# Performance work log

Hardware: AMD Instinct MI355X
Metric: run time of the kernel (lower is better)

Reference implementation:

```python
import math
import jax, jax.numpy as jnp
import numpy as np

EMBED_DIM = 192
N_HEADS = 6
WS = 7          # window size (hardcoded by RelativeEmbedding's 13x13 table)
HW = 56         # spatial height = width (N = 56*56 = 3136)
BATCH = 32
NW = HW // WS   # windows per side = 8
WW = WS * WS    # tokens per window = 49


def _rel_indices():
    # Replicates the from-scratch Swin RelativeEmbedding index construction:
    # x = arange(1, 8, 1/7); xi = trunc(x[None]-x[:,None]); y = tile(arange(1,8), 7)
    xs = np.arange(1.0, 8.0, 1.0 / 7.0)          # 49 values
    xi = (xs[None, :] - xs[:, None]).astype(np.int32)  # trunc toward zero, in [-6, 6]
    ys = np.concatenate([np.arange(1, 8)] * 7)
    yi = (ys[None, :] - ys[:, None]).astype(np.int32)
    # torch negative indexing wraps -> emulate with mod 13
    return jnp.asarray(xi % 13), jnp.asarray(yi % 13)


def _masks():
    half = WS * (WS // 2)  # 21
    mm = np.zeros((WW, WW), dtype=np.float32)
    mm[-half:, :-half] = -np.inf
    mm[:-half, -half:] = -np.inf
    # cross_mask = rearrange(mm, '(r w1) (c w2) -> (w1 r) (w2 c)')
    cross = mm.reshape(WS, WS, WS, WS).transpose(1, 0, 3, 2).reshape(WW, WW)
    return jnp.asarray(mm), jnp.asarray(cross)


def setup_inputs() -> dict:
    key = jax.random.key(0)
    ks = jax.random.split(key, 6)
    return {
        "x": jax.random.normal(ks[0], (BATCH, HW * HW, EMBED_DIM), jnp.float32),
        "W_qkv": jax.random.normal(ks[1], (3 * EMBED_DIM, EMBED_DIM), jnp.float32) * 0.02,
        "b_qkv": jax.random.normal(ks[2], (3 * EMBED_DIM,), jnp.float32) * 0.02,
        "W_out": jax.random.normal(ks[3], (EMBED_DIM, EMBED_DIM), jnp.float32) * 0.02,
        "b_out": jax.random.normal(ks[4], (EMBED_DIM,), jnp.float32) * 0.02,
        "B_rel": jax.random.normal(ks[5], (2 * WS - 1, 2 * WS - 1), jnp.float32),
    }


def reference(x, W_qkv, b_qkv, W_out, b_out, B_rel):
    B = x.shape[0]
    hd = EMBED_DIM // N_HEADS
    xi, yi = _rel_indices()
    bias = B_rel[xi, yi]                      # (49, 49) relative position bias
    mm, cross = _masks()

    qkv = x @ W_qkv.T + b_qkv                 # (B, N, 3E)
    # 'b (h w) (c k) -> b h w c k' : channel-major, k fastest
    qkv = qkv.reshape(B, HW, HW, EMBED_DIM, 3)
    # shifted windows: source uses -window_size // 2 == -4 (asymmetric w/ reverse +3)
    qkv = jnp.roll(qkv, shift=(-(WS) // 2, -(WS) // 2), axis=(1, 2))
    # 'b (h m1) (w m2) (H E) K -> b H h w (m1 m2) E K'
    qkv = qkv.reshape(B, NW, WS, NW, WS, N_HEADS, hd, 3)
    qkv = qkv.transpose(0, 5, 1, 3, 2, 4, 6, 7).reshape(B, N_HEADS, NW, NW, WW, hd, 3)
    q, k, v = qkv[..., 0], qkv[..., 1], qkv[..., 2]

    scores = jnp.einsum('bHhwie,bHhwje->bHhwij', q, k) / math.sqrt(hd)
    scores = scores + bias                    # broadcast over (b, H, h, w)
    # shift masking: last row of windows and last column of windows
    scores = scores.at[:, :, -1, :].add(mm)
    scores = scores.at[:, :, :, -1].add(cross)

    p = jax.nn.softmax(scores, axis=-1)
    out = jnp.einsum('bHhwij,bHhwje->bHhwie', p, v)  # (B, H, nw, nw, 49, hd)
    # 'b H h w (m1 m2) E -> b (h m1) (w m2) (H E)'
    out = out.reshape(B, N_HEADS, NW, NW, WS, WS, hd)
    out = out.transpose(0, 2, 4, 3, 5, 1, 6).reshape(B, HW, HW, EMBED_DIM)
    out = jnp.roll(out, shift=(WS // 2, WS // 2), axis=(1, 2))
    out = out.reshape(B, HW * HW, EMBED_DIM)
    return out @ W_out.T + b_out
```

## Files before the change

### kernel.cpp

```cpp
#include <hip/hip_runtime.h>

typedef _Float16 f16;
typedef _Float16 f16x4 __attribute__((ext_vector_type(4)));
typedef _Float16 f16x8 __attribute__((ext_vector_type(8)));
typedef float f32x4 __attribute__((ext_vector_type(4)));

#define MFMA32(A, B, C) __builtin_amdgcn_mfma_f32_16x16x32_f16((A), (B), (C), 0, 0, 0)
#if __has_builtin(__builtin_amdgcn_mfma_f32_16x16x16_f16)
#define MFMA16(A, B, C) __builtin_amdgcn_mfma_f32_16x16x16_f16((A), (B), (C), 0, 0, 0)
#else
#define MFMA16(A, B, C) __builtin_amdgcn_mfma_f32_16x16x16f16((A), (B), (C), 0, 0, 0)
#endif

__global__ void prep_kernel(const float* __restrict__ Wq, const float* __restrict__ bqkv,
                            const float* __restrict__ Wo, const float* __restrict__ Brel,
                            f16* __restrict__ wqd, f16* __restrict__ wod,
                            float* __restrict__ bqd, f16* __restrict__ biasreg) {
  int tid = blockIdx.x * blockDim.x + threadIdx.x;
  int nthr = gridDim.x * blockDim.x;
  for (int i = tid; i < 3 * 192 * 192; i += nthr) {
    int c = i % 192, n = (i / 192) % 192, kk = i / (192 * 192);
    wqd[i] = (f16)Wq[(size_t)(n * 3 + kk) * 192 + c];
  }
  for (int i = tid; i < 192 * 192; i += nthr) wod[i] = (f16)Wo[i];
  for (int i = tid; i < 3 * 192; i += nthr) {
    int n = i % 192, kk = i / 192;
    bqd[i] = bqkv[n * 3 + kk];
  }
  for (int idx = tid; idx < 4 * 4 * 4 * 64 * 4; idx += nthr) {
    int m = idx & 3, lane = (idx >> 2) & 63, jt = (idx >> 8) & 3,
        itt = (idx >> 10) & 3, t = idx >> 12;
    int i = itt * 16 + (lane & 15);
    int j = jt * 16 + 4 * (lane >> 4) + m;
    float v = -60000.0f;
    if (i < 49 && j < 49) {
      bool msk = false;
      if (t & 2) msk |= ((i / 7 >= 4) != (j / 7 >= 4));
      if (t & 1) msk |= ((i % 7 >= 4) != (j % 7 >= 4));
      if (!msk) {
        volatile double one = 1.0;
        volatile double step = 1.0 / 7.0;
        volatile double b1 = one + step;
        volatile double delta = b1 - one;
        volatile double mj = (double)j * delta;
        volatile double sj = 1.0 + mj;
        volatile double mi = (double)i * delta;
        volatile double si = 1.0 + mi;
        double d = (double)sj - (double)si;
        int xd = (int)d;
        int yd = (j % 7) - (i % 7);
        int xm = ((xd % 13) + 13) % 13;
        int ym = ((yd % 13) + 13) % 13;
        v = Brel[xm * 13 + ym];
      }
    }
    biasreg[idx] = (f16)v;
  }
}

__launch_bounds__(768, 3)
__global__ void swin_kernel(const float* __restrict__ x,
                            const float* __restrict__ bqd,
                            const float* __restrict__ bout,
                            const f16* __restrict__ wqd,
                            const f16* __restrict__ wod,
                            const f16* __restrict__ biasreg,
                            float* __restrict__ out) {
  __shared__ __align__(16) unsigned char xsm[2 * 64 * 384];

  const int tid = threadIdx.x;
  const int bid = blockIdx.x;
  const int p  = bid >> 6;
  const int wh = (bid >> 3) & 7;
  const int ww = bid & 7;
  const int lane = tid & 63;
  const int wv = tid >> 6;
  const int t  = (wv >= 6) ? 1 : 0;
  const int hd = wv - 6 * t;
  const int lr = lane & 15;
  const int lg = lane >> 4;

#define XP(tt, row, cb) ((void*)(xsm + (tt) * 24576 + (row) * 384 + ((cb) ^ (((row) & 7) << 4))))

  {
    for (int idx = tid; idx < 2 * 49 * 48; idx += 768) {
      int tw = idx / (49 * 48), r = idx % (49 * 48);
      int tok = r / 48, c4 = r % 48;
      const float* xb = x + (size_t)(2 * p + tw) * (3136 * 192);
      int m1 = tok / 7, m2 = tok % 7;
      int y  = wh * 7 + m1 + 4; if (y  >= 56) y  -= 56;
      int xx = ww * 7 + m2 + 4; if (xx >= 56) xx -= 56;
      float4 v = *(const float4*)(xb + ((y * 56 + xx) * 192 + c4 * 4));
      f16x4 h = { (f16)v.x, (f16)v.y, (f16)v.z, (f16)v.w };
      *(f16x4*)XP(tw, tok, c4 * 8) = h;
    }
    for (int idx = tid; idx < 2 * 15 * 24; idx += 768) {
      int tw = idx / (15 * 24), r = idx % (15 * 24);
      int tok = 49 + r / 24, c8 = r % 24;
      f16x8 z = {};
      *(f16x8*)XP(tw, tok, c8 * 16) = z;
    }
  }
  __syncthreads();

  f16x4 br[4][4];
  {
    int msk = ((wh == 7) ? 2 : 0) | ((ww == 7) ? 1 : 0);
    #pragma unroll
    for (int itt = 0; itt < 4; ++itt)
      #pragma unroll
      for (int jt = 0; jt < 4; ++jt)
        br[itt][jt] = *(const f16x4*)(biasreg + ((((msk * 4 + itt) * 4 + jt) * 64 + lane) * 4));
  }

  f16x4 qtf[2][4], ktf[2][4];
  {
    f32x4 qacc[2][4], kacc[2][4];
    #pragma unroll
    for (int nt = 0; nt < 2; ++nt)
      #pragma unroll
      for (int it = 0; it < 4; ++it) {
        qacc[nt][it] = (f32x4){0.f, 0.f, 0.f, 0.f};
        kacc[nt][it] = (f32x4){0.f, 0.f, 0.f, 0.f};
      }
    #pragma unroll
    for (int ks = 0; ks < 6; ++ks) {
      f16x8 a[4];
      #pragma unroll
      for (int it = 0; it < 4; ++it)
        a[it] = *(const f16x8*)XP(t, it * 16 + lr, ks * 64 + lg * 16);
      #pragma unroll
      for (int nt = 0; nt < 2; ++nt) {
        const size_t roff = (size_t)(hd * 32 + nt * 16 + lr) * 192 + ks * 32 + lg * 8;
        f16x8 wqf = *(const f16x8*)(wqd + roff);
        f16x8 wkf = *(const f16x8*)(wqd + 192 * 192 + roff);
        #pragma unroll
        for (int it = 0; it < 4; ++it) {
          qacc[nt][it] = MFMA32(wqf, a[it], qacc[nt][it]);
          kacc[nt][it] = MFMA32(wkf, a[it], kacc[nt][it]);
        }
      }
    }
    const float SCALE = 0.17677669529663687f;
    #pragma unroll
    for (int nt = 0; nt < 2; ++nt) {
      float4 bq4 = *(const float4*)(bqd + hd * 32 + nt * 16 + 4 * lg);
      float4 bk4 = *(const float4*)(bqd + 192 + hd * 32 + nt * 16 + 4 * lg);
      #pragma unroll
      for (int it = 0; it < 4; ++it) {
        f16x4 q, k;
        q[0] = (f16)((qacc[nt][it][0] + bq4.x) * SCALE);
        q[1] = (f16)((qacc[nt][it][1] + bq4.y) * SCALE);
        q[2] = (f16)((qacc[nt][it][2] + bq4.z) * SCALE);
        q[3] = (f16)((qacc[nt][it][3] + bq4.w) * SCALE);
        k[0] = (f16)(kacc[nt][it][0] + bk4.x);
        k[1] = (f16)(kacc[nt][it][1] + bk4.y);
        k[2] = (f16)(kacc[nt][it][2] + bk4.z);
        k[3] = (f16)(kacc[nt][it][3] + bk4.w);
        qtf[nt][it] = q; ktf[nt][it] = k;
      }
    }
  }

  f32x4 sacc[4][4];
  #pragma unroll
  for (int jt = 0; jt < 4; ++jt)
    #pragma unroll
    for (int it = 0; it < 4; ++it) {
      f32x4 c = (f32x4){0.f, 0.f, 0.f, 0.f};
      c = MFMA16(ktf[0][jt], qtf[0][it], c);
      sacc[jt][it] = MFMA16(ktf[1][jt], qtf[1][it], c);
    }

  f16x4 paf[4][4];
  #pragma unroll
  for (int itt = 0; itt < 4; ++itt) {
    float sv[16];
    #pragma unroll
    for (int jt = 0; jt < 4; ++jt)
      #pragma unroll
      for (int m = 0; m < 4; ++m)
        sv[jt * 4 + m] = sacc[jt][itt][m] + (float)br[itt][jt][m];
    float mx = sv[0];
    #pragma unroll
    for (int q = 1; q < 16; ++q) mx = fmaxf(mx, sv[q]);
    mx = fmaxf(mx, __shfl_xor(mx, 16));
    mx = fmaxf(mx, __shfl_xor(mx, 32));
    float sum = 0.f;
    #pragma unroll
    for (int q = 0; q < 16; ++q) { sv[q] = __expf(sv[q] - mx); sum += sv[q]; }
    sum += __shfl_xor(sum, 16);
    sum += __shfl_xor(sum, 32);
    float rv = 1.0f / sum;
    #pragma unroll
    for (int jt = 0; jt < 4; ++jt) {
      f16x4 pk = { (f16)(sv[jt*4+0] * rv), (f16)(sv[jt*4+1] * rv),
                   (f16)(sv[jt*4+2] * rv), (f16)(sv[jt*4+3] * rv) };
      paf[jt][itt] = pk;
    }
  }

  f16x4 vf[4][2];
  {
    f32x4 vacc[4][2];
    #pragma unroll
    for (int jt = 0; jt < 4; ++jt)
      #pragma unroll
      for (int et = 0; et < 2; ++et)
        vacc[jt][et] = (f32x4){0.f, 0.f, 0.f, 0.f};
    #pragma unroll
    for (int ks = 0; ks < 6; ++ks) {
      f16x8 a[4];
      #pragma unroll
      for (int jt = 0; jt < 4; ++jt)
        a[jt] = *(const f16x8*)XP(t, jt * 16 + lr, ks * 64 + lg * 16);
      #pragma unroll
      for (int et = 0; et < 2; ++et) {
        f16x8 wvf = *(const f16x8*)(wqd + 2 * 192 * 192 +
                      (size_t)(hd * 32 + et * 16 + lr) * 192 + ks * 32 + lg * 8);
        #pragma unroll
        for (int jt = 0; jt < 4; ++jt)
          vacc[jt][et] = MFMA32(a[jt], wvf, vacc[jt][et]);
      }
    }
    #pragma unroll
    for (int et = 0; et < 2; ++et) {
      float bv = bqd[2 * 192 + hd * 32 + et * 16 + lr];
      #pragma unroll
      for (int jt = 0; jt < 4; ++jt) {
        f16x4 v;
        #pragma unroll
        for (int m = 0; m < 4; ++m) v[m] = (f16)(vacc[jt][et][m] + bv);
        vf[jt][et] = v;
      }
    }
  }

  f32x4 oacc[4][2];
  #pragma unroll
  for (int it = 0; it < 4; ++it)
    #pragma unroll
    for (int et = 0; et < 2; ++et) {
      f32x4 c = (f32x4){0.f, 0.f, 0.f, 0.f};
      #pragma unroll
      for (int jt = 0; jt < 4; ++jt)
        c = MFMA16(paf[jt][it], vf[jt][et], c);
      oacc[it][et] = c;
    }

  __syncthreads();

  #pragma unroll
  for (int it = 0; it < 4; ++it)
    #pragma unroll
    for (int et = 0; et < 2; ++et)
      #pragma unroll
      for (int m = 0; m < 4; ++m) {
        int i = it * 16 + 4 * lg + m;
        *(f16*)XP(t, i, hd * 64 + et * 32 + lr * 2) = (f16)(oacc[it][et][m]);
      }
  __syncthreads();

  f32x4 zacc[2][4];
  {
    #pragma unroll
    for (int nt = 0; nt < 2; ++nt)
      #pragma unroll
      for (int it = 0; it < 4; ++it)
        zacc[nt][it] = (f32x4){0.f, 0.f, 0.f, 0.f};
    #pragma unroll
    for (int ks = 0; ks < 6; ++ks) {
      f16x8 a[4];
      #pragma unroll
      for (int it = 0; it < 4; ++it)
        a[it] = *(const f16x8*)XP(t, it * 16 + lr, ks * 64 + lg * 16);
      #pragma unroll
      for (int nt = 0; nt < 2; ++nt) {
        f16x8 bw = *(const f16x8*)(wod + (size_t)(hd * 32 + nt * 16 + lr) * 192 + ks * 32 + lg * 8);
        #pragma unroll
        for (int it = 0; it < 4; ++it)
          zacc[nt][it] = MFMA32(a[it], bw, zacc[nt][it]);
      }
    }
  }
  __syncthreads();

  #pragma unroll
  for (int nt = 0; nt < 2; ++nt) {
    int n = hd * 32 + nt * 16 + lr;
    float bo = bout[n];
    #pragma unroll
    for (int it = 0; it < 4; ++it)
      #pragma unroll
      for (int m = 0; m < 4; ++m) {
        int i = it * 16 + 4 * lg + m;
        *(f16*)XP(t, i, n * 2) = (f16)(zacc[nt][it][m] + bo);
      }
  }
  __syncthreads();

  {
    for (int idx = tid; idx < 2 * 49 * 48; idx += 768) {
      int tw = idx / (49 * 48), r = idx % (49 * 48);
      int tok = r / 48, c4 = r % 48;
      float* outb = out + (size_t)(2 * p + tw) * (3136 * 192);
      f16x4 z = *(const f16x4*)XP(tw, tok, c4 * 8);
      int m1 = tok / 7, m2 = tok % 7;
      int y  = wh * 7 + m1 + 3; if (y  >= 56) y  -= 56;
      int xx = ww * 7 + m2 + 3; if (xx >= 56) xx -= 56;
      float4 v = { (float)z[0], (float)z[1], (float)z[2], (float)z[3] };
      *(float4*)(outb + (size_t)(y * 56 + xx) * 192 + c4 * 4) = v;
    }
  }
#undef XP
}

extern "C" void kernel_launch(void* const* d_in, const int* in_sizes, int n_in,
                              void* d_out, int out_size, void* d_ws, size_t ws_size,
                              hipStream_t stream) {
  const float* x    = (const float*)d_in[0];
  const float* Wq   = (const float*)d_in[1];
  const float* bq   = (const float*)d_in[2];
  const float* Wo   = (const float*)d_in[3];
  const float* bo   = (const float*)d_in[4];
  const float* Brel = (const float*)d_in[5];

  f16*   wqd     = (f16*)d_ws;
  f16*   wod     = (f16*)((char*)d_ws + 0x38000);
  float* bqd     = (float*)((char*)d_ws + 0x4A000);
  f16*   biasreg = (f16*)((char*)d_ws + 0x4B000);

  hipLaunchKernelGGL(prep_kernel, dim3(256), dim3(256), 0, stream,
                     Wq, bq, Wo, Brel, wqd, wod, bqd, biasreg);
  hipLaunchKernelGGL(swin_kernel, dim3(16 * 8 * 8), dim3(768), 0, stream,
                     x, bqd, bo, wqd, wod, biasreg, (float*)d_out);
}
```

Baseline: 155.7 us.

## Warp-specialize swin kernel with dedicated load/store waves double-buffering window pairs

The grid is reduced to 256 persistent-style blocks of 1024 threads. Each block handles four image pairs for one window position. Twelve compute waves run attention, while four extra waves store the previous pair's output and prefetch the next pair into a second LDS buffer. Global loads and stores also become nontemporal. The aim is to hide the gather/scatter memory latency behind MFMA work, at the cost of double the LDS (96KB per block), fewer blocks in flight, and the matching __syncthreads counts that the producer waves rely on.

```diff
diff --git a/kernel.cpp b/kernel.cpp
--- a/kernel.cpp
+++ b/kernel.cpp
@@ -58,7 +58,7 @@
   }
 }
 
-__launch_bounds__(768, 3)
+__launch_bounds__(1024, 4)
 __global__ void swin_kernel(const float* __restrict__ x,
                             const float* __restrict__ bqd,
                             const float* __restrict__ bout,
@@ -66,41 +66,63 @@
                             const f16* __restrict__ wod,
                             const f16* __restrict__ biasreg,
                             float* __restrict__ out) {
-  __shared__ __align__(16) unsigned char xsm[2 * 64 * 384];
+  __shared__ __align__(16) unsigned char xsm[4 * 64 * 384];
 
   const int tid = threadIdx.x;
   const int bid = blockIdx.x;
-  const int p  = bid >> 6;
   const int wh = (bid >> 3) & 7;
   const int ww = bid & 7;
+  const int g  = bid >> 6;
   const int lane = tid & 63;
   const int wv = tid >> 6;
-  const int t  = (wv >= 6) ? 1 : 0;
-  const int hd = wv - 6 * t;
+  const bool isC = (wv < 12);
+  const int t  = (isC && wv >= 6) ? 1 : 0;
+  const int hd = isC ? (wv - 6 * t) : 0;
   const int lr = lane & 15;
   const int lg = lane >> 4;
+  const int mid = (wv - 12) * 64 + lane;
 
 #define XP(tt, row, cb) ((void*)(xsm + (tt) * 24576 + (row) * 384 + ((cb) ^ (((row) & 7) << 4))))
 
-  {
-    for (int idx = tid; idx < 2 * 49 * 48; idx += 768) {
-      int tw = idx / (49 * 48), r = idx % (49 * 48);
-      int tok = r / 48, c4 = r % 48;
-      const float* xb = x + (size_t)(2 * p + tw) * (3136 * 192);
-      int m1 = tok / 7, m2 = tok % 7;
-      int y  = wh * 7 + m1 + 4; if (y  >= 56) y  -= 56;
-      int xx = ww * 7 + m2 + 4; if (xx >= 56) xx -= 56;
-      float4 v = *(const float4*)(xb + ((y * 56 + xx) * 192 + c4 * 4));
-      f16x4 h = { (f16)v.x, (f16)v.y, (f16)v.z, (f16)v.w };
-      *(f16x4*)XP(tw, tok, c4 * 8) = h;
-    }
-    for (int idx = tid; idx < 2 * 15 * 24; idx += 768) {
-      int tw = idx / (15 * 24), r = idx % (15 * 24);
-      int tok = 49 + r / 24, c8 = r % 24;
-      f16x8 z = {};
-      *(f16x8*)XP(tw, tok, c8 * 16) = z;
-    }
-  }
+#define STAGE(pr, st, base, stride)                                              \
+  {                                                                              \
+    for (int idx = (base); idx < 4704; idx += (stride)) {                        \
+      int tw = idx / 2352, r = idx % 2352;                                       \
+      int tok = r / 48, c4 = r % 48;                                             \
+      const float* xb = x + (size_t)(2 * (pr) + tw) * (3136 * 192);              \
+      int m1 = tok / 7, m2 = tok % 7;                                            \
+      int y  = wh * 7 + m1 + 4; if (y  >= 56) y  -= 56;                          \
+      int xx = ww * 7 + m2 + 4; if (xx >= 56) xx -= 56;                          \
+      f32x4 v = __builtin_nontemporal_load(                                      \
+          (const f32x4*)(xb + ((y * 56 + xx) * 192 + c4 * 4)));                  \
+      f16x4 h = { (f16)v[0], (f16)v[1], (f16)v[2], (f16)v[3] };                  \
+      *(f16x4*)XP((st) * 2 + tw, tok, c4 * 8) = h;                               \
+    }                                                                            \
+    for (int idx = (base); idx < 720; idx += (stride)) {                         \
+      int tw = idx / 360, r = idx % 360;                                         \
+      int tok = 49 + r / 24, c8 = r % 24;                                        \
+      f16x8 z = {};                                                              \
+      *(f16x8*)XP((st) * 2 + tw, tok, c8 * 16) = z;                              \
+    }                                                                            \
+  }
+
+#define EPILOGUE(pr, st, base, stride)                                           \
+  {                                                                              \
+    for (int idx = (base); idx < 4704; idx += (stride)) {                        \
+      int tw = idx / 2352, r = idx % 2352;                                       \
+      int tok = r / 48, c4 = r % 48;                                             \
+      float* outb = out + (size_t)(2 * (pr) + tw) * (3136 * 192);                \
+      f16x4 z = *(const f16x4*)XP((st) * 2 + tw, tok, c4 * 8);                   \
+      int m1 = tok / 7, m2 = tok % 7;                                            \
+      int y  = wh * 7 + m1 + 3; if (y  >= 56) y  -= 56;                          \
+      int xx = ww * 7 + m2 + 3; if (xx >= 56) xx -= 56;                          \
+      f32x4 v = { (float)z[0], (float)z[1], (float)z[2], (float)z[3] };          \
+      __builtin_nontemporal_store(v,                                             \
+          (f32x4*)(outb + (size_t)(y * 56 + xx) * 192 + c4 * 4));                \
+    }                                                                            \
+  }
+
+  STAGE(g * 4, 0, tid, 1024)
   __syncthreads();
 
   f16x4 br[4][4];
@@ -113,206 +135,210 @@
         br[itt][jt] = *(const f16x4*)(biasreg + ((((msk * 4 + itt) * 4 + jt) * 64 + lane) * 4));
   }
 
-  f16x4 qtf[2][4], ktf[2][4];
-  {
-    f32x4 qacc[2][4], kacc[2][4];
-    #pragma unroll
-    for (int nt = 0; nt < 2; ++nt)
-      #pragma unroll
-      for (int it = 0; it < 4; ++it) {
-        qacc[nt][it] = (f32x4){0.f, 0.f, 0.f, 0.f};
-        kacc[nt][it] = (f32x4){0.f, 0.f, 0.f, 0.f};
-      }
-    #pragma unroll
-    for (int ks = 0; ks < 6; ++ks) {
-      f16x8 a[4];
+  for (int w = 0; w < 4; ++w) {
+    const int S = w & 1;
+    const int tt = S * 2 + t;
+
+    if (isC) {
+      f16x4 qtf[2][4], ktf[2][4];
+      {
+        f32x4 qacc[2][4], kacc[2][4];
+        #pragma unroll
+        for (int nt = 0; nt < 2; ++nt)
+          #pragma unroll
+          for (int it = 0; it < 4; ++it) {
+            qacc[nt][it] = (f32x4){0.f, 0.f, 0.f, 0.f};
+            kacc[nt][it] = (f32x4){0.f, 0.f, 0.f, 0.f};
+          }
+        #pragma unroll
+        for (int ks = 0; ks < 6; ++ks) {
+          f16x8 a[4];
+          #pragma unroll
+          for (int it = 0; it < 4; ++it)
+            a[it] = *(const f16x8*)XP(tt, it * 16 + lr, ks * 64 + lg * 16);
+          #pragma unroll
+          for (int nt = 0; nt < 2; ++nt) {
+            const size_t roff = (size_t)(hd * 32 + nt * 16 + lr) * 192 + ks * 32 + lg * 8;
+            f16x8 wqf = *(const f16x8*)(wqd + roff);
+            f16x8 wkf = *(const f16x8*)(wqd + 192 * 192 + roff);
+            #pragma unroll
+            for (int it = 0; it < 4; ++it) {
+              qacc[nt][it] = MFMA32(wqf, a[it], qacc[nt][it]);
+              kacc[nt][it] = MFMA32(wkf, a[it], kacc[nt][it]);
+            }
+          }
+        }
+        const float SCALE = 0.17677669529663687f;
+        #pragma unroll
+        for (int nt = 0; nt < 2; ++nt) {
+          float4 bq4 = *(const float4*)(bqd + hd * 32 + nt * 16 + 4 * lg);
+          float4 bk4 = *(const float4*)(bqd + 192 + hd * 32 + nt * 16 + 4 * lg);
+          #pragma unroll
+          for (int it = 0; it < 4; ++it) {
+            f16x4 q, k;
+            q[0] = (f16)((qacc[nt][it][0] + bq4.x) * SCALE);
+            q[1] = (f16)((qacc[nt][it][1] + bq4.y) * SCALE);
+            q[2] = (f16)((qacc[nt][it][2] + bq4.z) * SCALE);
+            q[3] = (f16)((qacc[nt][it][3] + bq4.w) * SCALE);
+            k[0] = (f16)(kacc[nt][it][0] + bk4.x);
+            k[1] = (f16)(kacc[nt][it][1] + bk4.y);
+            k[2] = (f16)(kacc[nt][it][2] + bk4.z);
+            k[3] = (f16)(kacc[nt][it][3] + bk4.w);
+            qtf[nt][it] = q; ktf[nt][it] = k;
+          }
+        }
+      }
+
+      f32x4 sacc[4][4];
+      #pragma unroll
+      for (int jt = 0; jt < 4; ++jt)
+        #pragma unroll
+        for (int it = 0; it < 4; ++it) {
+          f32x4 c = (f32x4){0.f, 0.f, 0.f, 0.f};
+          c = MFMA16(ktf[0][jt], qtf[0][it], c);
+          sacc[jt][it] = MFMA16(ktf[1][jt], qtf[1][it], c);
+        }
+
+      f16x4 paf[4][4];
+      #pragma unroll
+      for (int itt = 0; itt < 4; ++itt) {
+        float sv[16];
+        #pragma unroll
+        for (int jt = 0; jt < 4; ++jt)
+          #pragma unroll
+          for (int m = 0; m < 4; ++m)
+            sv[jt * 4 + m] = sacc[jt][itt][m] + (float)br[itt][jt][m];
+        float mx = sv[0];
+        #pragma unroll
+        for (int q = 1; q < 16; ++q) mx = fmaxf(mx, sv[q]);
+        mx = fmaxf(mx, __shfl_xor(mx, 16));
+        mx = fmaxf(mx, __shfl_xor(mx, 32));
+        float sum = 0.f;
+        #pragma unroll
+        for (int q = 0; q < 16; ++q) { sv[q] = __expf(sv[q] - mx); sum += sv[q]; }
+        sum += __shfl_xor(sum, 16);
+        sum += __shfl_xor(sum, 32);
+        float rv = 1.0f / sum;
+        #pragma unroll
+        for (int jt = 0; jt < 4; ++jt) {
+          f16x4 pk = { (f16)(sv[jt*4+0] * rv), (f16)(sv[jt*4+1] * rv),
+                       (f16)(sv[jt*4+2] * rv), (f16)(sv[jt*4+3] * rv) };
+          paf[jt][itt] = pk;
+        }
+      }
+
+      f16x4 vf[4][2];
+      {
+        f32x4 vacc[4][2];
+        #pragma unroll
+        for (int jt = 0; jt < 4; ++jt)
+          #pragma unroll
+          for (int et = 0; et < 2; ++et)
+            vacc[jt][et] = (f32x4){0.f, 0.f, 0.f, 0.f};
+        #pragma unroll
+        for (int ks = 0; ks < 6; ++ks) {
+          f16x8 a[4];
+          #pragma unroll
+          for (int jt = 0; jt < 4; ++jt)
+            a[jt] = *(const f16x8*)XP(tt, jt * 16 + lr, ks * 64 + lg * 16);
+          #pragma unroll
+          for (int et = 0; et < 2; ++et) {
+            f16x8 wvf = *(const f16x8*)(wqd + 2 * 192 * 192 +
+                          (size_t)(hd * 32 + et * 16 + lr) * 192 + ks * 32 + lg * 8);
+            #pragma unroll
+            for (int jt = 0; jt < 4; ++jt)
+              vacc[jt][et] = MFMA32(a[jt], wvf, vacc[jt][et]);
+          }
+        }
+        #pragma unroll
+        for (int et = 0; et < 2; ++et) {
+          float bv = bqd[2 * 192 + hd * 32 + et * 16 + lr];
+          #pragma unroll
+          for (int jt = 0; jt < 4; ++jt) {
+            f16x4 v;
+            #pragma unroll
+            for (int m = 0; m < 4; ++m) v[m] = (f16)(vacc[jt][et][m] + bv);
+            vf[jt][et] = v;
+          }
+        }
+      }
+
+      f32x4 oacc[4][2];
       #pragma unroll
       for (int it = 0; it < 4; ++it)
-        a[it] = *(const f16x8*)XP(t, it * 16 + lr, ks * 64 + lg * 16);
+        #pragma unroll
+        for (int et = 0; et < 2; ++et) {
+          f32x4 c = (f32x4){0.f, 0.f, 0.f, 0.f};
+          #pragma unroll
+          for (int jt = 0; jt < 4; ++jt)
+            c = MFMA16(paf[jt][it], vf[jt][et], c);
+          oacc[it][et] = c;
+        }
+
+      __syncthreads();
+
+      #pragma unroll
+      for (int it = 0; it < 4; ++it)
+        #pragma unroll
+        for (int et = 0; et < 2; ++et)
+          #pragma unroll
+          for (int m = 0; m < 4; ++m) {
+            int i = it * 16 + 4 * lg + m;
+            *(f16*)XP(tt, i, hd * 64 + et * 32 + lr * 2) = (f16)(oacc[it][et][m]);
+          }
+      __syncthreads();
+
+      f32x4 zacc[2][4];
+      {
+        #pragma unroll
+        for (int nt = 0; nt < 2; ++nt)
+          #pragma unroll
+          for (int it = 0; it < 4; ++it)
+            zacc[nt][it] = (f32x4){0.f, 0.f, 0.f, 0.f};
+        #pragma unroll
+        for (int ks = 0; ks < 6; ++ks) {
+          f16x8 a[4];
+          #pragma unroll
+          for (int it = 0; it < 4; ++it)
+            a[it] = *(const f16x8*)XP(tt, it * 16 + lr, ks * 64 + lg * 16);
+          #pragma unroll
+          for (int nt = 0; nt < 2; ++nt) {
+            f16x8 bw = *(const f16x8*)(wod + (size_t)(hd * 32 + nt * 16 + lr) * 192 + ks * 32 + lg * 8);
+            #pragma unroll
+            for (int it = 0; it < 4; ++it)
+              zacc[nt][it] = MFMA32(a[it], bw, zacc[nt][it]);
+          }
+        }
+      }
+      __syncthreads();
+
       #pragma unroll
       for (int nt = 0; nt < 2; ++nt) {
-        const size_t roff = (size_t)(hd * 32 + nt * 16 + lr) * 192 + ks * 32 + lg * 8;
-        f16x8 wqf = *(const f16x8*)(wqd + roff);
-        f16x8 wkf = *(const f16x8*)(wqd + 192 * 192 + roff);
-        #pragma unroll
-        for (int it = 0; it < 4; ++it) {
-          qacc[nt][it] = MFMA32(wqf, a[it], qacc[nt][it]);
-          kacc[nt][it] = MFMA32(wkf, a[it], kacc[nt][it]);
-        }
-      }
+        int n = hd * 32 + nt * 16 + lr;
+        float bo = bout[n];
+        #pragma unroll
+        for (int it = 0; it < 4; ++it)
+          #pragma unroll
+          for (int m = 0; m < 4; ++m) {
+            int i = it * 16 + 4 * lg + m;
+            *(f16*)XP(tt, i, n * 2) = (f16)(zacc[nt][it][m] + bo);
+          }
+      }
+      __syncthreads();
+    } else {
+      if (w > 0) EPILOGUE(g * 4 + w - 1, S ^ 1, mid, 256)
+      if (w < 3) STAGE(g * 4 + w + 1, S ^ 1, mid, 256)
+      __syncthreads();
+      __syncthreads();
+      __syncthreads();
+      __syncthreads();
     }
-    const float SCALE = 0.17677669529663687f;
-    #pragma unroll
-    for (int nt = 0; nt < 2; ++nt) {
-      float4 bq4 = *(const float4*)(bqd + hd * 32 + nt * 16 + 4 * lg);
-      float4 bk4 = *(const float4*)(bqd + 192 + hd * 32 + nt * 16 + 4 * lg);
-      #pragma unroll
-      for (int it = 0; it < 4; ++it) {
-        f16x4 q, k;
-        q[0] = (f16)((qacc[nt][it][0] + bq4.x) * SCALE);
-        q[1] = (f16)((qacc[nt][it][1] + bq4.y) * SCALE);
-        q[2] = (f16)((qacc[nt][it][2] + bq4.z) * SCALE);
-        q[3] = (f16)((qacc[nt][it][3] + bq4.w) * SCALE);
-        k[0] = (f16)(kacc[nt][it][0] + bk4.x);
-        k[1] = (f16)(kacc[nt][it][1] + bk4.y);
-        k[2] = (f16)(kacc[nt][it][2] + bk4.z);
-        k[3] = (f16)(kacc[nt][it][3] + bk4.w);
-        qtf[nt][it] = q; ktf[nt][it] = k;
-      }
-    }
-  }
-
-  f32x4 sacc[4][4];
-  #pragma unroll
-  for (int jt = 0; jt < 4; ++jt)
-    #pragma unroll
-    for (int it = 0; it < 4; ++it) {
-      f32x4 c = (f32x4){0.f, 0.f, 0.f, 0.f};
-      c = MFMA16(ktf[0][jt], qtf[0][it], c);
-      sacc[jt][it] = MFMA16(ktf[1][jt], qtf[1][it], c);
-    }
-
-  f16x4 paf[4][4];
-  #pragma unroll
-  for (int itt = 0; itt < 4; ++itt) {
-    float sv[16];
-    #pragma unroll
-    for (int jt = 0; jt < 4; ++jt)
-      #pragma unroll
-      for (int m = 0; m < 4; ++m)
-        sv[jt * 4 + m] = sacc[jt][itt][m] + (float)br[itt][jt][m];
-    float mx = sv[0];
-    #pragma unroll
-    for (int q = 1; q < 16; ++q) mx = fmaxf(mx, sv[q]);
-    mx = fmaxf(mx, __shfl_xor(mx, 16));
-    mx = fmaxf(mx, __shfl_xor(mx, 32));
-    float sum = 0.f;
-    #pragma unroll
-    for (int q = 0; q < 16; ++q) { sv[q] = __expf(sv[q] - mx); sum += sv[q]; }
-    sum += __shfl_xor(sum, 16);
-    sum += __shfl_xor(sum, 32);
-    float rv = 1.0f / sum;
-    #pragma unroll
-    for (int jt = 0; jt < 4; ++jt) {
-      f16x4 pk = { (f16)(sv[jt*4+0] * rv), (f16)(sv[jt*4+1] * rv),
-                   (f16)(sv[jt*4+2] * rv), (f16)(sv[jt*4+3] * rv) };
-      paf[jt][itt] = pk;
-    }
-  }
-
-  f16x4 vf[4][2];
-  {
-    f32x4 vacc[4][2];
-    #pragma unroll
-    for (int jt = 0; jt < 4; ++jt)
-      #pragma unroll
-      for (int et = 0; et < 2; ++et)
-        vacc[jt][et] = (f32x4){0.f, 0.f, 0.f, 0.f};
-    #pragma unroll
-    for (int ks = 0; ks < 6; ++ks) {
-      f16x8 a[4];
-      #pragma unroll
-      for (int jt = 0; jt < 4; ++jt)
-        a[jt] = *(const f16x8*)XP(t, jt * 16 + lr, ks * 64 + lg * 16);
-      #pragma unroll
-      for (int et = 0; et < 2; ++et) {
-        f16x8 wvf = *(const f16x8*)(wqd + 2 * 192 * 192 +
-                      (size_t)(hd * 32 + et * 16 + lr) * 192 + ks * 32 + lg * 8);
-        #pragma unroll
-        for (int jt = 0; jt < 4; ++jt)
-          vacc[jt][et] = MFMA32(a[jt], wvf, vacc[jt][et]);
-      }
-    }
-    #pragma unroll
-    for (int et = 0; et < 2; ++et) {
-      float bv = bqd[2 * 192 + hd * 32 + et * 16 + lr];
-      #pragma unroll
-      for (int jt = 0; jt < 4; ++jt) {
-        f16x4 v;
-        #pragma unroll
-        for (int m = 0; m < 4; ++m) v[m] = (f16)(vacc[jt][et][m] + bv);
-        vf[jt][et] = v;
-      }
-    }
-  }
-
-  f32x4 oacc[4][2];
-  #pragma unroll
-  for (int it = 0; it < 4; ++it)
-    #pragma unroll
-    for (int et = 0; et < 2; ++et) {
-      f32x4 c = (f32x4){0.f, 0.f, 0.f, 0.f};
-      #pragma unroll
-      for (int jt = 0; jt < 4; ++jt)
-        c = MFMA16(paf[jt][it], vf[jt][et], c);
-      oacc[it][et] = c;
-    }
-
-  __syncthreads();
-
-  #pragma unroll
-  for (int it = 0; it < 4; ++it)
-    #pragma unroll
-    for (int et = 0; et < 2; ++et)
-      #pragma unroll
-      for (int m = 0; m < 4; ++m) {
-        int i = it * 16 + 4 * lg + m;
-        *(f16*)XP(t, i, hd * 64 + et * 32 + lr * 2) = (f16)(oacc[it][et][m]);
-      }
-  __syncthreads();
-
-  f32x4 zacc[2][4];
-  {
-    #pragma unroll
-    for (int nt = 0; nt < 2; ++nt)
-      #pragma unroll
-      for (int it = 0; it < 4; ++it)
-        zacc[nt][it] = (f32x4){0.f, 0.f, 0.f, 0.f};
-    #pragma unroll
-    for (int ks = 0; ks < 6; ++ks) {
-      f16x8 a[4];
-      #pragma unroll
-      for (int it = 0; it < 4; ++it)
-        a[it] = *(const f16x8*)XP(t, it * 16 + lr, ks * 64 + lg * 16);
-      #pragma unroll
-      for (int nt = 0; nt < 2; ++nt) {
-        f16x8 bw = *(const f16x8*)(wod + (size_t)(hd * 32 + nt * 16 + lr) * 192 + ks * 32 + lg * 8);
-        #pragma unroll
-        for (int it = 0; it < 4; ++it)
-          zacc[nt][it] = MFMA32(a[it], bw, zacc[nt][it]);
-      }
-    }
-  }
-  __syncthreads();
-
-  #pragma unroll
-  for (int nt = 0; nt < 2; ++nt) {
-    int n = hd * 32 + nt * 16 + lr;
-    float bo = bout[n];
-    #pragma unroll
-    for (int it = 0; it < 4; ++it)
-      #pragma unroll
-      for (int m = 0; m < 4; ++m) {
-        int i = it * 16 + 4 * lg + m;
-        *(f16*)XP(t, i, n * 2) = (f16)(zacc[nt][it][m] + bo);
-      }
-  }
-  __syncthreads();
-
-  {
-    for (int idx = tid; idx < 2 * 49 * 48; idx += 768) {
-      int tw = idx / (49 * 48), r = idx % (49 * 48);
-      int tok = r / 48, c4 = r % 48;
-      float* outb = out + (size_t)(2 * p + tw) * (3136 * 192);
-      f16x4 z = *(const f16x4*)XP(tw, tok, c4 * 8);
-      int m1 = tok / 7, m2 = tok % 7;
-      int y  = wh * 7 + m1 + 3; if (y  >= 56) y  -= 56;
-      int xx = ww * 7 + m2 + 3; if (xx >= 56) xx -= 56;
-      float4 v = { (float)z[0], (float)z[1], (float)z[2], (float)z[3] };
-      *(float4*)(outb + (size_t)(y * 56 + xx) * 192 + c4 * 4) = v;
-    }
-  }
+  }
+
+  EPILOGUE(g * 4 + 3, 1, tid, 1024)
 #undef XP
+#undef STAGE
+#undef EPILOGUE
 }
 
 extern "C" void kernel_launch(void* const* d_in, const int* in_sizes, int n_in,
@@ -332,6 +358,6 @@
 
   hipLaunchKernelGGL(prep_kernel, dim3(256), dim3(256), 0, stream,
                      Wq, bq, Wo, Brel, wqd, wod, bqd, biasreg);
-  hipLaunchKernelGGL(swin_kernel, dim3(16 * 8 * 8), dim3(768), 0, stream,
+  hipLaunchKernelGGL(swin_kernel, dim3(256), dim3(1024), 0, stream,
                      x, bqd, bo, wqd, wod, biasreg, (float*)d_out);
 }
```

Result: slower. 411.6 us (+164.4%).
